# Kernel optimization log

Hardware: AMD Instinct MI355X
Metric: run time of the kernel (lower is better)

Reference implementation:

```python
import jax, jax.numpy as jnp
import numpy as np

F = 16          # features
C = 128         # context features
H = 256         # conditioner hidden
L = 8           # coupling layers
K = 8           # spline bins
TB = 3.0        # tail bound
T = F // 2      # transform features per layer (8)
PDIM = 3 * K - 1  # params per transformed feature (23), tails='linear'
MIN_W = MIN_H = MIN_D = 1e-3
B = 65536


def _feature_split(layer):
    ev = np.arange(0, F, 2)
    od = np.arange(1, F, 2)
    tr, idn = (ev, od) if layer % 2 == 0 else (od, ev)  # mask>0 => transform
    inv = np.argsort(np.concatenate([idn, tr]))
    return idn, tr, inv


def _rq_spline(x, uw, uh, ud):
    """Monotonic rational-quadratic spline with linear tails (nflows semantics).
    x: [B,T]; uw/uh: [B,T,K]; ud: [B,T,K-1]. Returns (y, logabsdet) per element."""
    const = np.log(np.expm1(1.0 - MIN_D))  # pad value so boundary derivative == 1
    ud = jnp.pad(ud, ((0, 0), (0, 0), (1, 1)), constant_values=const)  # [B,T,K+1]
    inside = (x >= -TB) & (x <= TB)
    xs = jnp.clip(x, -TB, TB)

    w = jax.nn.softmax(uw, axis=-1)
    w = MIN_W + (1.0 - MIN_W * K) * w
    cw = jnp.pad(jnp.cumsum(w, -1), ((0, 0), (0, 0), (1, 0)))
    cw = 2.0 * TB * cw - TB
    cw = cw.at[..., 0].set(-TB).at[..., -1].set(TB)
    w = cw[..., 1:] - cw[..., :-1]

    d = MIN_D + jax.nn.softplus(ud)  # [B,T,K+1]

    h = jax.nn.softmax(uh, axis=-1)
    h = MIN_H + (1.0 - MIN_H * K) * h
    ch = jnp.pad(jnp.cumsum(h, -1), ((0, 0), (0, 0), (1, 0)))
    ch = 2.0 * TB * ch - TB
    ch = ch.at[..., 0].set(-TB).at[..., -1].set(TB)
    h = ch[..., 1:] - ch[..., :-1]

    # bin search on cumulative widths (forward direction)
    idx = jnp.clip(jnp.sum((xs[..., None] >= cw).astype(jnp.int32), -1) - 1, 0, K - 1)
    g = lambda a: jnp.take_along_axis(a, idx[..., None], axis=-1)[..., 0]

    x0, bw = g(cw[..., :K]), g(w)
    y0, bh = g(ch[..., :K]), g(h)
    delta = g(h / w)
    d0, d1 = g(d[..., :K]), g(d[..., 1:])

    th = (xs - x0) / bw
    th1m = th * (1.0 - th)
    num = bh * (delta * th * th + d0 * th1m)
    den = delta + (d0 + d1 - 2.0 * delta) * th1m
    y = y0 + num / den
    dnum = delta * delta * (d1 * th * th + 2.0 * delta * th1m + d0 * (1.0 - th) ** 2)
    ld = jnp.log(dnum) - 2.0 * jnp.log(den)
    return jnp.where(inside, y, x), jnp.where(inside, ld, 0.0)


def setup_inputs() -> dict:
    key = jax.random.key(0)
    ks = jax.random.split(key, 8)
    inputs = jax.random.normal(ks[0], (B, F), jnp.float32)
    context = jax.random.normal(ks[1], (B, C), jnp.float32)
    s = lambda k, shape, fan: jax.random.normal(k, shape, jnp.float32) / np.sqrt(fan)
    W1 = s(ks[2], (L, T + C, H), T + C)
    b1 = jnp.zeros((L, H), jnp.float32)
    W2 = s(ks[3], (L, H, H), H)
    b2 = jnp.zeros((L, H), jnp.float32)
    W3 = s(ks[4], (L, H, T * PDIM), H)
    b3 = jnp.zeros((L, T * PDIM), jnp.float32)
    rng = np.random.default_rng(0)  # fixed-at-init RandomPermutation buffers
    perms = jnp.asarray(np.stack([rng.permutation(F) for _ in range(L - 1)]), jnp.int32)
    return dict(inputs=inputs, context=context, W1=W1, b1=b1, W2=W2, b2=b2,
                W3=W3, b3=b3, perms=perms)


def reference(inputs, context, W1, b1, W2, b2, W3, b3, perms):
    x = jnp.clip(inputs, -1.0, 1.0)
    logdet = jnp.zeros(x.shape[0], x.dtype)
    for i in range(L):
        idn, tr, inv = _feature_split(i)
        xi = x[:, idn]
        xt = x[:, tr]
        hdn = jax.nn.relu(jnp.concatenate([xi, context], -1) @ W1[i] + b1[i])
        hdn = jax.nn.relu(hdn @ W2[i] + b2[i])
        p = (hdn @ W3[i] + b3[i]).reshape(-1, T, PDIM)
        yt, ld = _rq_spline(xt, p[..., :K], p[..., K:2 * K], p[..., 2 * K:])
        x = jnp.concatenate([xi, yt], -1)[:, inv]
        logdet = logdet + jnp.sum(ld, -1)
        if i < L - 1:
            x = x[:, perms[i]]
    return jnp.clip(x, -1.0, 1.0), logdet
```

## Files before the change

kernel.cpp:

```cpp
#include <hip/hip_runtime.h>
#include <math.h>

#define BATCH 65536
#define FDIM 16
#define CDIM 128
#define HDIM 256
#define NL 8
#define KBINS 8
#define TDIM 8
#define PD 23
#define TBV 3.0f
#define K1 160
#define N3 184
#define N3P 192
#define PSTR 197
#define MR 64
#define XSTR 40

typedef _Float16 f16;
typedef __attribute__((ext_vector_type(8))) _Float16 f16x8;
typedef __attribute__((ext_vector_type(4))) float f32x4;

__global__ __launch_bounds__(256)
void conv_w1_kernel(const float* __restrict__ W1,
                    f16* __restrict__ Wh, f16* __restrict__ Wl) {
    int idx = blockIdx.x * 256 + threadIdx.x;
    if (idx >= NL * HDIM * K1) return;
    int l = idx / (HDIM * K1);
    int rem = idx - l * (HDIM * K1);
    int n = rem / K1;
    int k = rem - n * K1;
    int row = (k < 128) ? (8 + k) : ((k < 136) ? (k - 128) : -1);
    float v = (row >= 0) ? W1[((size_t)l * 136 + row) * HDIM + n] : 0.f;
    f16 hv = (f16)v;
    Wh[idx] = hv; Wl[idx] = (f16)(v - (float)hv);
}

__global__ __launch_bounds__(256)
void conv_w2_kernel(const float* __restrict__ W2,
                    f16* __restrict__ Wh, f16* __restrict__ Wl) {
    int idx = blockIdx.x * 256 + threadIdx.x;
    if (idx >= NL * HDIM * HDIM) return;
    int l = idx / (HDIM * HDIM);
    int rem = idx - l * (HDIM * HDIM);
    int n = rem >> 8;
    int k = rem & 255;
    float v = W2[((size_t)l * HDIM + k) * HDIM + n];
    f16 hv = (f16)v;
    Wh[idx] = hv; Wl[idx] = (f16)(v - (float)hv);
}

__global__ __launch_bounds__(256)
void conv_w3_kernel(const float* __restrict__ W3,
                    f16* __restrict__ Wh, f16* __restrict__ Wl) {
    int idx = blockIdx.x * 256 + threadIdx.x;
    if (idx >= NL * N3P * HDIM) return;
    int l = idx / (N3P * HDIM);
    int rem = idx - l * (N3P * HDIM);
    int n = rem >> 8;
    int k = rem & 255;
    float v = (n < N3) ? W3[((size_t)l * HDIM + k) * N3 + n] : 0.f;
    f16 hv = (f16)v;
    Wh[idx] = hv; Wl[idx] = (f16)(v - (float)hv);
}

__global__ __launch_bounds__(256)
void conv_ctx_kernel(const float* __restrict__ ctx,
                     f16* __restrict__ ch, f16* __restrict__ cl) {
    size_t idx = ((size_t)blockIdx.x * 256 + threadIdx.x) * 4;
    if (idx >= (size_t)BATCH * CDIM) return;
    float4 v = *(const float4*)&ctx[idx];
    f16 h;
    h = (f16)v.x; ch[idx + 0] = h; cl[idx + 0] = (f16)(v.x - (float)h);
    h = (f16)v.y; ch[idx + 1] = h; cl[idx + 1] = (f16)(v.y - (float)h);
    h = (f16)v.z; ch[idx + 2] = h; cl[idx + 2] = (f16)(v.z - (float)h);
    h = (f16)v.w; ch[idx + 3] = h; cl[idx + 3] = (f16)(v.w - (float)h);
}

__device__ __forceinline__ float softplusf(float v) {
    return fmaxf(v, 0.f) + log1pf(expf(-fabsf(v)));
}

__device__ __forceinline__ void gld16(const f16* src, f16* dst) {
    __builtin_amdgcn_global_load_lds(
        (const __attribute__((address_space(1))) unsigned int*)src,
        (__attribute__((address_space(3))) unsigned int*)dst, 16, 0, 0);
}

template<int N> __device__ __forceinline__ void vmw() {
    asm volatile("s_waitcnt vmcnt(%0)" :: "n"(N) : "memory");
    __builtin_amdgcn_sched_barrier(0);
}
__device__ __forceinline__ void barr() {
    __builtin_amdgcn_s_barrier();
    __builtin_amdgcn_sched_barrier(0);
}
__device__ __forceinline__ void lgkm_bar() {
    asm volatile("s_waitcnt lgkmcnt(0)" ::: "memory");
    __builtin_amdgcn_s_barrier();
    __builtin_amdgcn_sched_barrier(0);
}

__global__ __launch_bounds__(512, 1)
void flow_kernel(const float* __restrict__ in,
                 const f16* __restrict__ ctxh, const f16* __restrict__ ctxl,
                 const f16* __restrict__ W1h, const f16* __restrict__ W1l,
                 const f16* __restrict__ W2h, const f16* __restrict__ W2l,
                 const f16* __restrict__ W3h, const f16* __restrict__ W3l,
                 const float* __restrict__ b1, const float* __restrict__ b2,
                 const float* __restrict__ b3, const int* __restrict__ perms,
                 float* __restrict__ out) {
    __shared__ __align__(16) char arena[131072];
    __shared__ __align__(16) f16 sXi[2][MR * XSTR];
    __shared__ float sX[2][MR][17];
    __shared__ float sY[MR][9];
    __shared__ float sLd[MR][9];
    __shared__ float sLdet[MR];
    __shared__ float sBias[768];
    __shared__ int   sPerm[(NL - 1) * FDIM];

    f16* sH = (f16*)arena;
    float* sP = (float*)arena;

    const int tid = threadIdx.x;
    const int lane = tid & 63;
    const int w = tid >> 6;
    const int lr = lane & 15, lh = lane >> 4;
    const int bid = blockIdx.x;
    const int wgid = (bid & 7) * 32 + (bid >> 3);
    const int wcol0 = w * 32;
    const int bxor = (lh ^ (lr & 3)) << 4;

    char* const wbuf = arena + 32768 + w * 12288;

    auto stageB = [&](const f16* Wh, const f16* Wl, int b, int kt, int KD) {
        char* dst = wbuf + b * 4096;
        #pragma unroll
        for (int ii = 0; ii < 2; ++ii) {
            int si = ii * 64 + lane;
            int c = si >> 2, seg = si & 3;
            const f16* sh = Wh + (size_t)(wcol0 + c) * KD + kt * 32 + (seg ^ (c & 3)) * 8;
            const f16* sl = Wl + (size_t)(wcol0 + c) * KD + kt * 32 + (seg ^ (c & 3)) * 8;
            gld16(sh, (f16*)(dst + ii * 1024 + lane * 16));
            gld16(sl, (f16*)(dst + 2048 + ii * 1024 + lane * 16));
        }
    };

    for (int rb = 0; rb < 4; ++rb) {
        const int rbase = (rb * 256 + wgid) * MR;
        lgkm_bar();

        {
            int r = tid >> 3, c2 = (tid & 7) * 2;
            float2 v = *(const float2*)&in[(size_t)(rbase + r) * FDIM + c2];
            sX[0][r][c2 + 0] = fminf(fmaxf(v.x, -1.f), 1.f);
            sX[0][r][c2 + 1] = fminf(fmaxf(v.y, -1.f), 1.f);
        }
        if (tid < MR) sLdet[tid] = 0.f;
        if (rb == 0 && tid < (NL - 1) * FDIM) sPerm[tid] = perms[tid];

        int cur = 0;
        for (int l = 0; l < NL; ++l) {
            lgkm_bar();

            {
                float bv1 = (tid < 256) ? b1[l * HDIM + tid]
                                        : b2[l * HDIM + (tid - 256)];
                float bv3 = b3[l * N3 + (tid < N3 ? tid : N3 - 1)];
                sBias[tid] = bv1;
                if (tid < N3) sBias[512 + tid] = bv3;
            }
            if (tid < MR) {
                int r = tid, off = 1 - (l & 1);
                #pragma unroll
                for (int k = 0; k < 8; ++k) {
                    float v = sX[cur][r][2 * k + off];
                    f16 hv = (f16)v;
                    sXi[0][r * XSTR + k] = hv;
                    sXi[1][r * XSTR + k] = (f16)(v - (float)hv);
                }
                #pragma unroll
                for (int k = 8; k < 32; ++k) {
                    sXi[0][r * XSTR + k] = (f16)0.f;
                    sXi[1][r * XSTR + k] = (f16)0.f;
                }
            }
            #pragma unroll
            for (int s = 0; s < 4; ++s) {
                int slot = s * 512 + tid;
                int p = slot >> 10, sp = slot & 1023;
                int row = sp >> 4, blk = sp & 15;
                const f16* src = (p ? ctxl : ctxh)
                               + (size_t)(rbase + row) * CDIM + (blk ^ (row & 7)) * 8;
                gld16(src, (f16*)(arena + slot * 16));
            }
            const f16* W1hL = W1h + (size_t)l * HDIM * K1;
            const f16* W1lL = W1l + (size_t)l * HDIM * K1;
            const f16* W2hL = W2h + (size_t)l * HDIM * HDIM;
            const f16* W2lL = W2l + (size_t)l * HDIM * HDIM;
            const f16* W3hL = W3h + (size_t)l * N3P * HDIM;
            const f16* W3lL = W3l + (size_t)l * N3P * HDIM;
            stageB(W1hL, W1lL, 0, 0, K1);
            stageB(W1hL, W1lL, 1, 1, K1);
            vmw<8>();
            lgkm_bar();

            f32x4 acc[4][2];
            #pragma unroll
            for (int i = 0; i < 4; ++i)
                #pragma unroll
                for (int j = 0; j < 2; ++j) acc[i][j] = (f32x4){0.f, 0.f, 0.f, 0.f};
            #pragma unroll
            for (int kt = 0; kt < 5; ++kt) {
                if (kt < 3) stageB(W1hL, W1lL, (kt + 2) % 3, kt + 2, K1);
                if (kt < 3) vmw<8>(); else if (kt == 3) vmw<4>(); else vmw<0>();
                f16x8 ah[4], al[4];
                if (kt < 4) {
                    #pragma unroll
                    for (int i = 0; i < 4; ++i) {
                        int row = i * 16 + lr;
                        int byo = row * 256 + ((kt * 64 + lh * 16) ^ ((row & 7) << 4));
                        ah[i] = *(const f16x8*)(arena + byo);
                        al[i] = *(const f16x8*)(arena + 16384 + byo);
                    }
                } else {
                    #pragma unroll
                    for (int i = 0; i < 4; ++i) {
                        int row = i * 16 + lr;
                        ah[i] = *(const f16x8*)&sXi[0][row * XSTR + lh * 8];
                        al[i] = *(const f16x8*)&sXi[1][row * XSTR + lh * 8];
                    }
                }
                const char* bb = wbuf + (kt % 3) * 4096;
                __builtin_amdgcn_s_setprio(1);
                #pragma unroll
                for (int j = 0; j < 2; ++j) {
                    int cb = (j * 16 + lr) * 64 + bxor;
                    f16x8 bh = *(const f16x8*)(bb + cb);
                    f16x8 bl = *(const f16x8*)(bb + 2048 + cb);
                    #pragma unroll
                    for (int i = 0; i < 4; ++i) {
                        acc[i][j] = __builtin_amdgcn_mfma_f32_16x16x32_f16(ah[i], bh, acc[i][j], 0, 0, 0);
                        acc[i][j] = __builtin_amdgcn_mfma_f32_16x16x32_f16(ah[i], bl, acc[i][j], 0, 0, 0);
                        acc[i][j] = __builtin_amdgcn_mfma_f32_16x16x32_f16(al[i], bh, acc[i][j], 0, 0, 0);
                    }
                }
                __builtin_amdgcn_s_setprio(0);
                __builtin_amdgcn_sched_barrier(0);
            }
            barr();
            #pragma unroll
            for (int j = 0; j < 2; ++j) {
                int col = wcol0 + j * 16 + lr;
                float bv = sBias[col];
                #pragma unroll
                for (int i = 0; i < 4; ++i)
                    #pragma unroll
                    for (int q = 0; q < 4; ++q) {
                        float v = fmaxf(acc[i][j][q] + bv, 0.f);
                        int row = i * 16 + lh * 4 + q;
                        int e = ((row << 8) + col) ^ ((row & 7) << 3);
                        sH[e] = (f16)v;
                    }
            }
            stageB(W2hL, W2lL, 0, 0, HDIM);
            stageB(W2hL, W2lL, 1, 1, HDIM);
            lgkm_bar();

            #pragma unroll
            for (int i = 0; i < 4; ++i)
                #pragma unroll
                for (int j = 0; j < 2; ++j) acc[i][j] = (f32x4){0.f, 0.f, 0.f, 0.f};
            #pragma unroll
            for (int kt = 0; kt < 8; ++kt) {
                if (kt < 6) stageB(W2hL, W2lL, (kt + 2) % 3, kt + 2, HDIM);
                if (kt < 6) vmw<8>(); else if (kt == 6) vmw<4>(); else vmw<0>();
                int k0 = kt * 32 + lh * 8;
                f16x8 ah[4];
                #pragma unroll
                for (int i = 0; i < 4; ++i) {
                    int row = i * 16 + lr;
                    int e = ((row << 8) + k0) ^ ((row & 7) << 3);
                    ah[i] = *(const f16x8*)&sH[e];
                }
                const char* bb = wbuf + (kt % 3) * 4096;
                __builtin_amdgcn_s_setprio(1);
                #pragma unroll
                for (int j = 0; j < 2; ++j) {
                    int cb = (j * 16 + lr) * 64 + bxor;
                    f16x8 bh = *(const f16x8*)(bb + cb);
                    f16x8 bl = *(const f16x8*)(bb + 2048 + cb);
                    #pragma unroll
                    for (int i = 0; i < 4; ++i) {
                        acc[i][j] = __builtin_amdgcn_mfma_f32_16x16x32_f16(ah[i], bh, acc[i][j], 0, 0, 0);
                        acc[i][j] = __builtin_amdgcn_mfma_f32_16x16x32_f16(ah[i], bl, acc[i][j], 0, 0, 0);
                    }
                }
                __builtin_amdgcn_s_setprio(0);
                __builtin_amdgcn_sched_barrier(0);
            }
            barr();
            #pragma unroll
            for (int j = 0; j < 2; ++j) {
                int col = wcol0 + j * 16 + lr;
                float bv = sBias[256 + col];
                #pragma unroll
                for (int i = 0; i < 4; ++i)
                    #pragma unroll
                    for (int q = 0; q < 4; ++q) {
                        float v = fmaxf(acc[i][j][q] + bv, 0.f);
                        int row = i * 16 + lh * 4 + q;
                        int e = ((row << 8) + col) ^ ((row & 7) << 3);
                        sH[e] = (f16)v;
                    }
            }
            if (w < 6) {
                stageB(W3hL, W3lL, 0, 0, HDIM);
                stageB(W3hL, W3lL, 1, 1, HDIM);
            }
            lgkm_bar();

            f32x4 acc3[4][2];
            #pragma unroll
            for (int i = 0; i < 4; ++i)
                #pragma unroll
                for (int j = 0; j < 2; ++j) acc3[i][j] = (f32x4){0.f, 0.f, 0.f, 0.f};
            if (w < 6) {
                #pragma unroll
                for (int kt = 0; kt < 8; ++kt) {
                    if (kt < 6) stageB(W3hL, W3lL, (kt + 2) % 3, kt + 2, HDIM);
                    if (kt < 6) vmw<8>(); else if (kt == 6) vmw<4>(); else vmw<0>();
                    int k0 = kt * 32 + lh * 8;
                    f16x8 ah[4];
                    #pragma unroll
                    for (int i = 0; i < 4; ++i) {
                        int row = i * 16 + lr;
                        int e = ((row << 8) + k0) ^ ((row & 7) << 3);
                        ah[i] = *(const f16x8*)&sH[e];
                    }
                    const char* bb = wbuf + (kt % 3) * 4096;
                    __builtin_amdgcn_s_setprio(1);
                    #pragma unroll
                    for (int j = 0; j < 2; ++j) {
                        int cb = (j * 16 + lr) * 64 + bxor;
                        f16x8 bh = *(const f16x8*)(bb + cb);
                        f16x8 bl = *(const f16x8*)(bb + 2048 + cb);
                        #pragma unroll
                        for (int i = 0; i < 4; ++i) {
                            acc3[i][j] = __builtin_amdgcn_mfma_f32_16x16x32_f16(ah[i], bh, acc3[i][j], 0, 0, 0);
                            acc3[i][j] = __builtin_amdgcn_mfma_f32_16x16x32_f16(ah[i], bl, acc3[i][j], 0, 0, 0);
                        }
                    }
                    __builtin_amdgcn_s_setprio(0);
                    __builtin_amdgcn_sched_barrier(0);
                }
            }
            barr();
            if (w < 6) {
                #pragma unroll
                for (int j = 0; j < 2; ++j) {
                    int col = wcol0 + j * 16 + lr;
                    float bv = (col < N3) ? sBias[512 + col] : 0.f;
                    #pragma unroll
                    for (int i = 0; i < 4; ++i)
                        #pragma unroll
                        for (int q = 0; q < 4; ++q) {
                            int row = i * 16 + lh * 4 + q;
                            sP[row * PSTR + col] = acc3[i][j][q] + bv;
                        }
                }
            }
            lgkm_bar();

            {
                int r = tid & 63, t = tid >> 6;
                float xin = sX[cur][r][2 * t + (l & 1)];
                const float* pp = &sP[r * PSTR + t * PD];
                bool inside = (xin >= -TBV) && (xin <= TBV);
                float xs = fminf(fmaxf(xin, -TBV), TBV);

                float e0, e1, e2, e3, e4, e5, e6, e7;
                {
                    float a0 = pp[0], a1 = pp[1], a2 = pp[2], a3 = pp[3];
                    float a4 = pp[4], a5 = pp[5], a6 = pp[6], a7 = pp[7];
                    float m = fmaxf(fmaxf(fmaxf(a0, a1), fmaxf(a2, a3)),
                                    fmaxf(fmaxf(a4, a5), fmaxf(a6, a7)));
                    e0 = expf(a0 - m); e1 = expf(a1 - m); e2 = expf(a2 - m); e3 = expf(a3 - m);
                    e4 = expf(a4 - m); e5 = expf(a5 - m); e6 = expf(a6 - m); e7 = expf(a7 - m);
                }
                float swv = ((e0 + e1) + (e2 + e3)) + ((e4 + e5) + (e6 + e7));
                float cwc = (1.f - 0.001f * KBINS) / swv;
                float x0 = -TBV, x1 = TBV;
                int idx = 0;
                bool done = false;
                {
                    float cs = 0.f;
                    float ee[7] = {e0, e1, e2, e3, e4, e5, e6};
                    #pragma unroll
                    for (int k = 0; k < 7; ++k) {
                        cs += 0.001f + cwc * ee[k];
                        float nxt = 2.f * TBV * cs - TBV;
                        bool ge = (xs >= nxt);
                        x0 = ge ? nxt : x0;
                        idx += ge ? 1 : 0;
                        x1 = (!ge && !done) ? nxt : x1;
                        done = done || !ge;
                    }
                }
                float y0 = -TBV, y1 = TBV;
                {
                    float a0 = pp[8], a1 = pp[9], a2 = pp[10], a3 = pp[11];
                    float a4 = pp[12], a5 = pp[13], a6 = pp[14], a7 = pp[15];
                    float m = fmaxf(fmaxf(fmaxf(a0, a1), fmaxf(a2, a3)),
                                    fmaxf(fmaxf(a4, a5), fmaxf(a6, a7)));
                    float f0 = expf(a0 - m), f1 = expf(a1 - m), f2 = expf(a2 - m), f3 = expf(a3 - m);
                    float f4 = expf(a4 - m), f5 = expf(a5 - m), f6 = expf(a6 - m), f7 = expf(a7 - m);
                    float shv = ((f0 + f1) + (f2 + f3)) + ((f4 + f5) + (f6 + f7));
                    float chc = (1.f - 0.001f * KBINS) / shv;
                    float cs = 0.f;
                    float ff[7] = {f0, f1, f2, f3, f4, f5, f6};
                    #pragma unroll
                    for (int k = 0; k < 7; ++k) {
                        cs += 0.001f + chc * ff[k];
                        float nxt = 2.f * TBV * cs - TBV;
                        y0 = (k < idx) ? nxt : y0;
                        y1 = (k == idx) ? nxt : y1;
                    }
                }
                float udm = pp[16 + (idx > 0 ? idx - 1 : 0)];
                float udp = pp[16 + (idx < 7 ? idx : 6)];
                float d0 = (idx > 0) ? 0.001f + softplusf(udm) : 1.f;
                float d1 = (idx < 7) ? 0.001f + softplusf(udp) : 1.f;

                float bw = x1 - x0, bh2 = y1 - y0;
                float delta = bh2 / bw;
                float th = (xs - x0) / bw;
                float th1m = th * (1.f - th);
                float num = bh2 * (delta * th * th + d0 * th1m);
                float den = delta + (d0 + d1 - 2.f * delta) * th1m;
                float y = y0 + num / den;
                float omth = 1.f - th;
                float dnum = delta * delta * (d1 * th * th + 2.f * delta * th1m + d0 * omth * omth);
                float ldv = logf(dnum) - 2.f * logf(den);
                sY[r][t] = inside ? y : xin;
                sLd[r][t] = inside ? ldv : 0.f;
            }
            lgkm_bar();

            {
                int r = tid >> 3, f0 = (tid & 7) * 2;
                if (l < NL - 1) {
                    #pragma unroll
                    for (int ff = 0; ff < 2; ++ff) {
                        int f = f0 + ff;
                        int g = sPerm[l * FDIM + f];
                        float v = ((g & 1) == (l & 1)) ? sY[r][g >> 1] : sX[cur][r][g];
                        sX[cur ^ 1][r][f] = v;
                    }
                    if (f0 == 0) {
                        float s = 0.f;
                        #pragma unroll
                        for (int t = 0; t < 8; ++t) s += sLd[r][t];
                        sLdet[r] += s;
                    }
                } else {
                    float ov[2];
                    #pragma unroll
                    for (int ff = 0; ff < 2; ++ff) {
                        int f = f0 + ff;
                        float v = ((f & 1) == (l & 1)) ? sY[r][f >> 1] : sX[cur][r][f];
                        ov[ff] = fminf(fmaxf(v, -1.f), 1.f);
                    }
                    float2 o = {ov[0], ov[1]};
                    *(float2*)&out[(size_t)(rbase + r) * FDIM + f0] = o;
                    if (f0 == 0) {
                        float s = 0.f;
                        #pragma unroll
                        for (int t = 0; t < 8; ++t) s += sLd[r][t];
                        out[(size_t)BATCH * FDIM + rbase + r] = sLdet[r] + s;
                    }
                }
            }
            cur ^= 1;
        }
    }
}

extern "C" void kernel_launch(void* const* d_in, const int* in_sizes, int n_in,
                              void* d_out, int out_size, void* d_ws, size_t ws_size,
                              hipStream_t stream) {
    (void)in_sizes; (void)n_in; (void)out_size; (void)ws_size;
    const float* inputs  = (const float*)d_in[0];
    const float* context = (const float*)d_in[1];
    const float* W1 = (const float*)d_in[2];
    const float* b1 = (const float*)d_in[3];
    const float* W2 = (const float*)d_in[4];
    const float* b2 = (const float*)d_in[5];
    const float* W3 = (const float*)d_in[6];
    const float* b3 = (const float*)d_in[7];
    const int*   perms = (const int*)d_in[8];
    float* out = (float*)d_out;

    f16* W1h = (f16*)d_ws;
    f16* W1l = W1h + (size_t)NL * HDIM * K1;
    f16* W2h = W1l + (size_t)NL * HDIM * K1;
    f16* W2l = W2h + (size_t)NL * HDIM * HDIM;
    f16* W3h = W2l + (size_t)NL * HDIM * HDIM;
    f16* W3l = W3h + (size_t)NL * N3P * HDIM;
    f16* ctxh = W3l + (size_t)NL * N3P * HDIM;
    f16* ctxl = ctxh + (size_t)BATCH * CDIM;

    int n1 = NL * HDIM * K1;
    conv_w1_kernel<<<(n1 + 255) / 256, 256, 0, stream>>>(W1, W1h, W1l);
    int n2 = NL * HDIM * HDIM;
    conv_w2_kernel<<<(n2 + 255) / 256, 256, 0, stream>>>(W2, W2h, W2l);
    int n3 = NL * N3P * HDIM;
    conv_w3_kernel<<<(n3 + 255) / 256, 256, 0, stream>>>(W3, W3h, W3l);
    int nc = BATCH * CDIM / 4;
    conv_ctx_kernel<<<(nc + 255) / 256, 256, 0, stream>>>(context, ctxh, ctxl);

    flow_kernel<<<256, 512, 0, stream>>>(
        inputs, ctxh, ctxl, W1h, W1l, W2h, W2l, W3h, W3l,
        b1, b2, b3, perms, out);
}
```

Before: 588.2 us.

## Load weight fragments directly into registers and hoist context staging out of layer loop

Replaces the per-wave LDS staging of W1/W2/W3 tiles with direct global-to-register loads, double-buffered two k-steps ahead. Context rows are loaded into LDS once per row block instead of once per layer. Biases are read into registers instead of through a shared bias array, and the next layer's identity-feature fp16 split is written during the permutation step, which removes the separate prep pass and some barriers. In exchange, weight loads become strided global reads into VGPRs, which raises register pressure and makes the MFMA loop depend on global-memory latency.

```diff
diff --git a/kernel.cpp b/kernel.cpp
--- a/kernel.cpp
+++ b/kernel.cpp
@@ -110,17 +110,15 @@
                  const float* __restrict__ b1, const float* __restrict__ b2,
                  const float* __restrict__ b3, const int* __restrict__ perms,
                  float* __restrict__ out) {
-    __shared__ __align__(16) char arena[131072];
+    __shared__ __align__(16) f16 sCtx[2 * 8192];
+    __shared__ __align__(16) f16 sH[16384];
+    __shared__ __align__(16) float sPm[MR * PSTR];
     __shared__ __align__(16) f16 sXi[2][MR * XSTR];
     __shared__ float sX[2][MR][17];
     __shared__ float sY[MR][9];
     __shared__ float sLd[MR][9];
     __shared__ float sLdet[MR];
-    __shared__ float sBias[768];
     __shared__ int   sPerm[(NL - 1) * FDIM];
-
-    f16* sH = (f16*)arena;
-    float* sP = (float*)arena;
 
     const int tid = threadIdx.x;
     const int lane = tid & 63;
@@ -129,22 +127,6 @@
     const int bid = blockIdx.x;
     const int wgid = (bid & 7) * 32 + (bid >> 3);
     const int wcol0 = w * 32;
-    const int bxor = (lh ^ (lr & 3)) << 4;
-
-    char* const wbuf = arena + 32768 + w * 12288;
-
-    auto stageB = [&](const f16* Wh, const f16* Wl, int b, int kt, int KD) {
-        char* dst = wbuf + b * 4096;
-        #pragma unroll
-        for (int ii = 0; ii < 2; ++ii) {
-            int si = ii * 64 + lane;
-            int c = si >> 2, seg = si & 3;
-            const f16* sh = Wh + (size_t)(wcol0 + c) * KD + kt * 32 + (seg ^ (c & 3)) * 8;
-            const f16* sl = Wl + (size_t)(wcol0 + c) * KD + kt * 32 + (seg ^ (c & 3)) * 8;
-            gld16(sh, (f16*)(dst + ii * 1024 + lane * 16));
-            gld16(sl, (f16*)(dst + 2048 + ii * 1024 + lane * 16));
-        }
-    };
 
     for (int rb = 0; rb < 4; ++rb) {
         const int rbase = (rb * 256 + wgid) * MR;
@@ -153,75 +135,82 @@
         {
             int r = tid >> 3, c2 = (tid & 7) * 2;
             float2 v = *(const float2*)&in[(size_t)(rbase + r) * FDIM + c2];
-            sX[0][r][c2 + 0] = fminf(fmaxf(v.x, -1.f), 1.f);
-            sX[0][r][c2 + 1] = fminf(fmaxf(v.y, -1.f), 1.f);
+            float v0 = fminf(fmaxf(v.x, -1.f), 1.f);
+            float v1 = fminf(fmaxf(v.y, -1.f), 1.f);
+            sX[0][r][c2 + 0] = v0;
+            sX[0][r][c2 + 1] = v1;
+            f16 hx = (f16)v1;
+            sXi[0][r * XSTR + (tid & 7)] = hx;
+            sXi[1][r * XSTR + (tid & 7)] = (f16)(v1 - (float)hx);
         }
-        if (tid < MR) sLdet[tid] = 0.f;
+        if (tid < MR) {
+            sLdet[tid] = 0.f;
+            #pragma unroll
+            for (int k = 8; k < 32; ++k) {
+                sXi[0][tid * XSTR + k] = (f16)0.f;
+                sXi[1][tid * XSTR + k] = (f16)0.f;
+            }
+        }
         if (rb == 0 && tid < (NL - 1) * FDIM) sPerm[tid] = perms[tid];
+
+        #pragma unroll
+        for (int s = 0; s < 4; ++s) {
+            int slot = s * 512 + tid;
+            int p = slot >> 10, sp = slot & 1023;
+            int row = sp >> 4, blk = sp & 15;
+            const f16* src = (p ? ctxl : ctxh)
+                           + (size_t)(rbase + row) * CDIM + (blk ^ (row & 7)) * 8;
+            gld16(src, &sCtx[slot * 8]);
+        }
+        vmw<0>();
+        lgkm_bar();
 
         int cur = 0;
         for (int l = 0; l < NL; ++l) {
-            lgkm_bar();
-
-            {
-                float bv1 = (tid < 256) ? b1[l * HDIM + tid]
-                                        : b2[l * HDIM + (tid - 256)];
-                float bv3 = b3[l * N3 + (tid < N3 ? tid : N3 - 1)];
-                sBias[tid] = bv1;
-                if (tid < N3) sBias[512 + tid] = bv3;
-            }
-            if (tid < MR) {
-                int r = tid, off = 1 - (l & 1);
-                #pragma unroll
-                for (int k = 0; k < 8; ++k) {
-                    float v = sX[cur][r][2 * k + off];
-                    f16 hv = (f16)v;
-                    sXi[0][r * XSTR + k] = hv;
-                    sXi[1][r * XSTR + k] = (f16)(v - (float)hv);
-                }
-                #pragma unroll
-                for (int k = 8; k < 32; ++k) {
-                    sXi[0][r * XSTR + k] = (f16)0.f;
-                    sXi[1][r * XSTR + k] = (f16)0.f;
-                }
-            }
-            #pragma unroll
-            for (int s = 0; s < 4; ++s) {
-                int slot = s * 512 + tid;
-                int p = slot >> 10, sp = slot & 1023;
-                int row = sp >> 4, blk = sp & 15;
-                const f16* src = (p ? ctxl : ctxh)
-                               + (size_t)(rbase + row) * CDIM + (blk ^ (row & 7)) * 8;
-                gld16(src, (f16*)(arena + slot * 16));
-            }
+            if (l > 0) lgkm_bar();
+
             const f16* W1hL = W1h + (size_t)l * HDIM * K1;
             const f16* W1lL = W1l + (size_t)l * HDIM * K1;
             const f16* W2hL = W2h + (size_t)l * HDIM * HDIM;
             const f16* W2lL = W2l + (size_t)l * HDIM * HDIM;
             const f16* W3hL = W3h + (size_t)l * N3P * HDIM;
             const f16* W3lL = W3l + (size_t)l * N3P * HDIM;
-            stageB(W1hL, W1lL, 0, 0, K1);
-            stageB(W1hL, W1lL, 1, 1, K1);
-            vmw<8>();
-            lgkm_bar();
+
+            float bv1_0 = b1[l * HDIM + wcol0 + lr];
+            float bv1_1 = b1[l * HDIM + wcol0 + 16 + lr];
+            float bv2_0 = b2[l * HDIM + wcol0 + lr];
+            float bv2_1 = b2[l * HDIM + wcol0 + 16 + lr];
+            float bv3_0 = (w < 6 && wcol0 + lr < N3) ? b3[l * N3 + wcol0 + lr] : 0.f;
+            float bv3_1 = (w < 6 && wcol0 + 16 + lr < N3) ? b3[l * N3 + wcol0 + 16 + lr] : 0.f;
+
+            f16x8 bh[2][2], bl[2][2];
+
+            {
+                size_t o0 = (size_t)(wcol0 + lr) * K1 + lh * 8;
+                size_t o1 = o0 + (size_t)16 * K1;
+                bh[0][0] = *(const f16x8*)(W1hL + o0); bl[0][0] = *(const f16x8*)(W1lL + o0);
+                bh[0][1] = *(const f16x8*)(W1hL + o1); bl[0][1] = *(const f16x8*)(W1lL + o1);
+                bh[1][0] = *(const f16x8*)(W1hL + o0 + 32); bl[1][0] = *(const f16x8*)(W1lL + o0 + 32);
+                bh[1][1] = *(const f16x8*)(W1hL + o1 + 32); bl[1][1] = *(const f16x8*)(W1lL + o1 + 32);
+            }
 
             f32x4 acc[4][2];
             #pragma unroll
             for (int i = 0; i < 4; ++i)
                 #pragma unroll
                 for (int j = 0; j < 2; ++j) acc[i][j] = (f32x4){0.f, 0.f, 0.f, 0.f};
+
             #pragma unroll
             for (int kt = 0; kt < 5; ++kt) {
-                if (kt < 3) stageB(W1hL, W1lL, (kt + 2) % 3, kt + 2, K1);
-                if (kt < 3) vmw<8>(); else if (kt == 3) vmw<4>(); else vmw<0>();
+                const int pb = kt & 1;
                 f16x8 ah[4], al[4];
                 if (kt < 4) {
                     #pragma unroll
                     for (int i = 0; i < 4; ++i) {
                         int row = i * 16 + lr;
                         int byo = row * 256 + ((kt * 64 + lh * 16) ^ ((row & 7) << 4));
-                        ah[i] = *(const f16x8*)(arena + byo);
-                        al[i] = *(const f16x8*)(arena + 16384 + byo);
+                        ah[i] = *(const f16x8*)((const char*)sCtx + byo);
+                        al[i] = *(const f16x8*)((const char*)sCtx + 16384 + byo);
                     }
                 } else {
                     #pragma unroll
@@ -231,28 +220,27 @@
                         al[i] = *(const f16x8*)&sXi[1][row * XSTR + lh * 8];
                     }
                 }
-                const char* bb = wbuf + (kt % 3) * 4096;
                 __builtin_amdgcn_s_setprio(1);
                 #pragma unroll
-                for (int j = 0; j < 2; ++j) {
-                    int cb = (j * 16 + lr) * 64 + bxor;
-                    f16x8 bh = *(const f16x8*)(bb + cb);
-                    f16x8 bl = *(const f16x8*)(bb + 2048 + cb);
+                for (int j = 0; j < 2; ++j)
                     #pragma unroll
                     for (int i = 0; i < 4; ++i) {
-                        acc[i][j] = __builtin_amdgcn_mfma_f32_16x16x32_f16(ah[i], bh, acc[i][j], 0, 0, 0);
-                        acc[i][j] = __builtin_amdgcn_mfma_f32_16x16x32_f16(ah[i], bl, acc[i][j], 0, 0, 0);
-                        acc[i][j] = __builtin_amdgcn_mfma_f32_16x16x32_f16(al[i], bh, acc[i][j], 0, 0, 0);
-                    }
-                }
+                        acc[i][j] = __builtin_amdgcn_mfma_f32_16x16x32_f16(ah[i], bh[pb][j], acc[i][j], 0, 0, 0);
+                        acc[i][j] = __builtin_amdgcn_mfma_f32_16x16x32_f16(ah[i], bl[pb][j], acc[i][j], 0, 0, 0);
+                        acc[i][j] = __builtin_amdgcn_mfma_f32_16x16x32_f16(al[i], bh[pb][j], acc[i][j], 0, 0, 0);
+                    }
                 __builtin_amdgcn_s_setprio(0);
-                __builtin_amdgcn_sched_barrier(0);
-            }
-            barr();
+                if (kt + 2 < 5) {
+                    size_t o0 = (size_t)(wcol0 + lr) * K1 + (kt + 2) * 32 + lh * 8;
+                    size_t o1 = o0 + (size_t)16 * K1;
+                    bh[pb][0] = *(const f16x8*)(W1hL + o0); bl[pb][0] = *(const f16x8*)(W1lL + o0);
+                    bh[pb][1] = *(const f16x8*)(W1hL + o1); bl[pb][1] = *(const f16x8*)(W1lL + o1);
+                }
+            }
             #pragma unroll
             for (int j = 0; j < 2; ++j) {
                 int col = wcol0 + j * 16 + lr;
-                float bv = sBias[col];
+                float bv = j ? bv1_1 : bv1_0;
                 #pragma unroll
                 for (int i = 0; i < 4; ++i)
                     #pragma unroll
@@ -263,8 +251,14 @@
                         sH[e] = (f16)v;
                     }
             }
-            stageB(W2hL, W2lL, 0, 0, HDIM);
-            stageB(W2hL, W2lL, 1, 1, HDIM);
+            {
+                size_t o0 = (size_t)(wcol0 + lr) * HDIM + lh * 8;
+                size_t o1 = o0 + (size_t)16 * HDIM;
+                bh[0][0] = *(const f16x8*)(W2hL + o0); bl[0][0] = *(const f16x8*)(W2lL + o0);
+                bh[0][1] = *(const f16x8*)(W2hL + o1); bl[0][1] = *(const f16x8*)(W2lL + o1);
+                bh[1][0] = *(const f16x8*)(W2hL + o0 + 32); bl[1][0] = *(const f16x8*)(W2lL + o0 + 32);
+                bh[1][1] = *(const f16x8*)(W2hL + o1 + 32); bl[1][1] = *(const f16x8*)(W2lL + o1 + 32);
+            }
             lgkm_bar();
 
             #pragma unroll
@@ -273,8 +267,7 @@
                 for (int j = 0; j < 2; ++j) acc[i][j] = (f32x4){0.f, 0.f, 0.f, 0.f};
             #pragma unroll
             for (int kt = 0; kt < 8; ++kt) {
-                if (kt < 6) stageB(W2hL, W2lL, (kt + 2) % 3, kt + 2, HDIM);
-                if (kt < 6) vmw<8>(); else if (kt == 6) vmw<4>(); else vmw<0>();
+                const int pb = kt & 1;
                 int k0 = kt * 32 + lh * 8;
                 f16x8 ah[4];
                 #pragma unroll
@@ -283,27 +276,27 @@
                     int e = ((row << 8) + k0) ^ ((row & 7) << 3);
                     ah[i] = *(const f16x8*)&sH[e];
                 }
-                const char* bb = wbuf + (kt % 3) * 4096;
                 __builtin_amdgcn_s_setprio(1);
                 #pragma unroll
-                for (int j = 0; j < 2; ++j) {
-                    int cb = (j * 16 + lr) * 64 + bxor;
-                    f16x8 bh = *(const f16x8*)(bb + cb);
-                    f16x8 bl = *(const f16x8*)(bb + 2048 + cb);
+                for (int j = 0; j < 2; ++j)
                     #pragma unroll
                     for (int i = 0; i < 4; ++i) {
-                        acc[i][j] = __builtin_amdgcn_mfma_f32_16x16x32_f16(ah[i], bh, acc[i][j], 0, 0, 0);
-                        acc[i][j] = __builtin_amdgcn_mfma_f32_16x16x32_f16(ah[i], bl, acc[i][j], 0, 0, 0);
-                    }
-                }
+                        acc[i][j] = __builtin_amdgcn_mfma_f32_16x16x32_f16(ah[i], bh[pb][j], acc[i][j], 0, 0, 0);
+                        acc[i][j] = __builtin_amdgcn_mfma_f32_16x16x32_f16(ah[i], bl[pb][j], acc[i][j], 0, 0, 0);
+                    }
                 __builtin_amdgcn_s_setprio(0);
-                __builtin_amdgcn_sched_barrier(0);
+                if (kt + 2 < 8) {
+                    size_t o0 = (size_t)(wcol0 + lr) * HDIM + (kt + 2) * 32 + lh * 8;
+                    size_t o1 = o0 + (size_t)16 * HDIM;
+                    bh[pb][0] = *(const f16x8*)(W2hL + o0); bl[pb][0] = *(const f16x8*)(W2lL + o0);
+                    bh[pb][1] = *(const f16x8*)(W2hL + o1); bl[pb][1] = *(const f16x8*)(W2lL + o1);
+                }
             }
             barr();
             #pragma unroll
             for (int j = 0; j < 2; ++j) {
                 int col = wcol0 + j * 16 + lr;
-                float bv = sBias[256 + col];
+                float bv = j ? bv2_1 : bv2_0;
                 #pragma unroll
                 for (int i = 0; i < 4; ++i)
                     #pragma unroll
@@ -315,21 +308,24 @@
                     }
             }
             if (w < 6) {
-                stageB(W3hL, W3lL, 0, 0, HDIM);
-                stageB(W3hL, W3lL, 1, 1, HDIM);
+                size_t o0 = (size_t)(wcol0 + lr) * HDIM + lh * 8;
+                size_t o1 = o0 + (size_t)16 * HDIM;
+                bh[0][0] = *(const f16x8*)(W3hL + o0); bl[0][0] = *(const f16x8*)(W3lL + o0);
+                bh[0][1] = *(const f16x8*)(W3hL + o1); bl[0][1] = *(const f16x8*)(W3lL + o1);
+                bh[1][0] = *(const f16x8*)(W3hL + o0 + 32); bl[1][0] = *(const f16x8*)(W3lL + o0 + 32);
+                bh[1][1] = *(const f16x8*)(W3hL + o1 + 32); bl[1][1] = *(const f16x8*)(W3lL + o1 + 32);
             }
             lgkm_bar();
 
-            f32x4 acc3[4][2];
-            #pragma unroll
-            for (int i = 0; i < 4; ++i)
-                #pragma unroll
-                for (int j = 0; j < 2; ++j) acc3[i][j] = (f32x4){0.f, 0.f, 0.f, 0.f};
             if (w < 6) {
+                f32x4 acc3[4][2];
+                #pragma unroll
+                for (int i = 0; i < 4; ++i)
+                    #pragma unroll
+                    for (int j = 0; j < 2; ++j) acc3[i][j] = (f32x4){0.f, 0.f, 0.f, 0.f};
                 #pragma unroll
                 for (int kt = 0; kt < 8; ++kt) {
-                    if (kt < 6) stageB(W3hL, W3lL, (kt + 2) % 3, kt + 2, HDIM);
-                    if (kt < 6) vmw<8>(); else if (kt == 6) vmw<4>(); else vmw<0>();
+                    const int pb = kt & 1;
                     int k0 = kt * 32 + lh * 8;
                     f16x8 ah[4];
                     #pragma unroll
@@ -338,35 +334,32 @@
                         int e = ((row << 8) + k0) ^ ((row & 7) << 3);
                         ah[i] = *(const f16x8*)&sH[e];
                     }
-                    const char* bb = wbuf + (kt % 3) * 4096;
                     __builtin_amdgcn_s_setprio(1);
                     #pragma unroll
-                    for (int j = 0; j < 2; ++j) {
-                        int cb = (j * 16 + lr) * 64 + bxor;
-                        f16x8 bh = *(const f16x8*)(bb + cb);
-                        f16x8 bl = *(const f16x8*)(bb + 2048 + cb);
+                    for (int j = 0; j < 2; ++j)
                         #pragma unroll
                         for (int i = 0; i < 4; ++i) {
-                            acc3[i][j] = __builtin_amdgcn_mfma_f32_16x16x32_f16(ah[i], bh, acc3[i][j], 0, 0, 0);
-                            acc3[i][j] = __builtin_amdgcn_mfma_f32_16x16x32_f16(ah[i], bl, acc3[i][j], 0, 0, 0);
+                            acc3[i][j] = __builtin_amdgcn_mfma_f32_16x16x32_f16(ah[i], bh[pb][j], acc3[i][j], 0, 0, 0);
+                            acc3[i][j] = __builtin_amdgcn_mfma_f32_16x16x32_f16(ah[i], bl[pb][j], acc3[i][j], 0, 0, 0);
                         }
-                    }
                     __builtin_amdgcn_s_setprio(0);
-                    __builtin_amdgcn_sched_barrier(0);
-                }
-            }
-            barr();
-            if (w < 6) {
+                    if (kt + 2 < 8) {
+                        size_t o0 = (size_t)(wcol0 + lr) * HDIM + (kt + 2) * 32 + lh * 8;
+                        size_t o1 = o0 + (size_t)16 * HDIM;
+                        bh[pb][0] = *(const f16x8*)(W3hL + o0); bl[pb][0] = *(const f16x8*)(W3lL + o0);
+                        bh[pb][1] = *(const f16x8*)(W3hL + o1); bl[pb][1] = *(const f16x8*)(W3lL + o1);
+                    }
+                }
                 #pragma unroll
                 for (int j = 0; j < 2; ++j) {
                     int col = wcol0 + j * 16 + lr;
-                    float bv = (col < N3) ? sBias[512 + col] : 0.f;
+                    float bv = j ? bv3_1 : bv3_0;
                     #pragma unroll
                     for (int i = 0; i < 4; ++i)
                         #pragma unroll
                         for (int q = 0; q < 4; ++q) {
                             int row = i * 16 + lh * 4 + q;
-                            sP[row * PSTR + col] = acc3[i][j][q] + bv;
+                            sPm[row * PSTR + col] = acc3[i][j][q] + bv;
                         }
                 }
             }
@@ -375,7 +368,7 @@
             {
                 int r = tid & 63, t = tid >> 6;
                 float xin = sX[cur][r][2 * t + (l & 1)];
-                const float* pp = &sP[r * PSTR + t * PD];
+                const float* pp = &sPm[r * PSTR + t * PD];
                 bool inside = (xin >= -TBV) && (xin <= TBV);
                 float xs = fminf(fmaxf(xin, -TBV), TBV);
 
@@ -450,13 +443,19 @@
             {
                 int r = tid >> 3, f0 = (tid & 7) * 2;
                 if (l < NL - 1) {
+                    float vv[2];
                     #pragma unroll
                     for (int ff = 0; ff < 2; ++ff) {
                         int f = f0 + ff;
                         int g = sPerm[l * FDIM + f];
                         float v = ((g & 1) == (l & 1)) ? sY[r][g >> 1] : sX[cur][r][g];
                         sX[cur ^ 1][r][f] = v;
-                    }
+                        vv[ff] = v;
+                    }
+                    float vxi = vv[l & 1];
+                    f16 hx = (f16)vxi;
+                    sXi[0][r * XSTR + (tid & 7)] = hx;
+                    sXi[1][r * XSTR + (tid & 7)] = (f16)(vxi - (float)hx);
                     if (f0 == 0) {
                         float s = 0.f;
                         #pragma unroll
```

After: 636.0 us. +8.1%, slower.
